# Kernel tuning notes

Hardware: AMD Instinct MI355X
Metric: run time of the kernel (lower is better)

## Reference

```python
import jax, jax.numpy as jnp
import numpy as np

N_NODES = 100000
N_EDGES = 1600000
IN_CH, HID_CH, N_CLASS = 512, 128, 40


def setup_inputs() -> dict:
    key = jax.random.key(0)
    k1, k2, k3, k4 = jax.random.split(key, 4)
    x = jax.random.normal(k1, (N_NODES, IN_CH), dtype=jnp.float32)
    edge_index = jax.random.randint(k2, (2, N_EDGES), 0, N_NODES, dtype=jnp.int64)
    W1 = jax.random.normal(k3, (IN_CH, HID_CH), dtype=jnp.float32) * (1.0 / np.sqrt(IN_CH))
    b1 = jnp.zeros((HID_CH,), dtype=jnp.float32)
    W2 = jax.random.normal(k4, (HID_CH, N_CLASS), dtype=jnp.float32) * (1.0 / np.sqrt(HID_CH))
    b2 = jnp.zeros((N_CLASS,), dtype=jnp.float32)
    return {"x": x, "edge_index": edge_index, "W1": W1, "b1": b1, "W2": W2, "b2": b2}


def _gcn_conv(x, src, dst, norm, W, b, n_nodes):
    # transform then sparse normalized aggregation: out = D^-1/2 (A+I) D^-1/2 (x W) + b
    h = x @ W                                  # [N, out_ch]
    msg = h[src] * norm[:, None]               # gather + scale, [E+N, out_ch]
    return jax.ops.segment_sum(msg, dst, num_segments=n_nodes) + b


def reference(x, edge_index, W1, b1, W2, b2):
    n = x.shape[0]
    loop = jnp.arange(n, dtype=edge_index.dtype)
    src = jnp.concatenate([edge_index[0], loop])   # add self-loops
    dst = jnp.concatenate([edge_index[1], loop])
    deg = jax.ops.segment_sum(jnp.ones_like(src, dtype=x.dtype), dst, num_segments=n)
    dinv = jnp.where(deg > 0, jax.lax.rsqrt(deg), 0.0)
    norm = dinv[src] * dinv[dst]                   # symmetric normalization

    h = jax.nn.relu(_gcn_conv(x, src, dst, norm, W1, b1, n))
    # dropout(p=0.5, train=False) -> identity in eval mode
    logits = _gcn_conv(h, src, dst, norm, W2, b2, n)
    return jax.nn.log_softmax(logits, axis=1)
```

## Files before the change

kernel.cpp:

```cpp
#include <hip/hip_runtime.h>
#include <math.h>

#define IN_CH 512
#define HID 128
#define NCLASS 40
#define SCAN_CHUNK 2048
#define FILL_CHUNKS 2048

typedef __attribute__((ext_vector_type(8))) short short8;
typedef __attribute__((ext_vector_type(4))) float float4v;

static __device__ inline ushort f2bf(float f) {
    unsigned int u = __float_as_uint(f);
    u += 0x7fffu + ((u >> 16) & 1u);
    return (ushort)(u >> 16);
}
static __device__ inline float bf2f(ushort u) {
    return __uint_as_float(((unsigned int)u) << 16);
}
static __device__ inline float blo(unsigned int u) { return __uint_as_float(u << 16); }
static __device__ inline float bhi(unsigned int u) { return __uint_as_float(u & 0xffff0000u); }

__global__ void k_count(const int* __restrict__ dst, int E, int* __restrict__ cnt) {
    int i = blockIdx.x * blockDim.x + threadIdx.x;
    if (i < E) atomicAdd(&cnt[dst[i]], 1);
}

__global__ __launch_bounds__(256) void k_scan_local(const int* __restrict__ cnt,
                                                    int* __restrict__ rowptr,
                                                    int* __restrict__ blocksum, int n) {
    __shared__ int ssum[256];
    int b = blockIdx.x, t = threadIdx.x;
    int base = b * SCAN_CHUNK + t * 8;
    int v[8], s = 0;
    #pragma unroll
    for (int i = 0; i < 8; ++i) {
        int idx = base + i;
        v[i] = (idx < n) ? cnt[idx] : 0;
        s += v[i];
    }
    ssum[t] = s;
    __syncthreads();
    for (int off = 1; off < 256; off <<= 1) {
        int x = (t >= off) ? ssum[t - off] : 0;
        __syncthreads();
        ssum[t] += x;
        __syncthreads();
    }
    int run = ssum[t] - s;
    #pragma unroll
    for (int i = 0; i < 8; ++i) {
        int idx = base + i;
        if (idx < n) rowptr[idx] = run;
        run += v[i];
    }
    if (t == 255) blocksum[b] = ssum[255];
}

__global__ void k_scan_blocksums(int* blocksum, int nb) {
    if (threadIdx.x == 0 && blockIdx.x == 0) {
        int acc = 0;
        for (int i = 0; i < nb; ++i) { int v = blocksum[i]; blocksum[i] = acc; acc += v; }
    }
}

__global__ void k_scan_add_dinv(int* __restrict__ rowptr, int* __restrict__ cursor,
                                const int* __restrict__ blocksum,
                                const int* __restrict__ cnt,
                                float* __restrict__ dinv, int n) {
    int i = blockIdx.x * blockDim.x + threadIdx.x;
    if (i < n) {
        int r = rowptr[i] + blocksum[i / SCAN_CHUNK];
        rowptr[i] = r;
        cursor[i] = r;
        dinv[i] = rsqrtf((float)cnt[i] + 1.0f);
    }
}

__global__ __launch_bounds__(256) void k_fill(const int* __restrict__ src,
                                              const int* __restrict__ dst,
                                              int* __restrict__ cursor,
                                              int* __restrict__ col, int E, int N) {
    int chunk = blockIdx.x;
    int e0 = (int)((long long)E * chunk / FILL_CHUNKS);
    int e1 = (int)((long long)E * (chunk + 1) / FILL_CHUNKS);
    int e = e0 + threadIdx.x;
    int s0 = 0, d0 = -1, s1 = 0, d1 = -1, s2 = 0, d2 = -1, s3 = 0, d3 = -1;
    if (e < e1)       { s0 = src[e];       d0 = dst[e]; }
    if (e + 256 < e1) { s1 = src[e + 256]; d1 = dst[e + 256]; }
    if (e + 512 < e1) { s2 = src[e + 512]; d2 = dst[e + 512]; }
    if (e + 768 < e1) { s3 = src[e + 768]; d3 = dst[e + 768]; }
    #pragma unroll
    for (int r = 0; r < 8; ++r) {
        int r0 = (N >> 3) * r;
        int r1 = (r == 7) ? N : r0 + (N >> 3);
        if (d0 >= r0 && d0 < r1) { int p = atomicAdd(&cursor[d0], 1); col[p] = s0; }
        if (d1 >= r0 && d1 < r1) { int p = atomicAdd(&cursor[d1], 1); col[p] = s1; }
        if (d2 >= r0 && d2 < r1) { int p = atomicAdd(&cursor[d2], 1); col[p] = s2; }
        if (d3 >= r0 && d3 < r1) { int p = atomicAdd(&cursor[d3], 1); col[p] = s3; }
    }
}

__global__ void k_wt(const float* __restrict__ W1, const float* __restrict__ W2,
                     ushort* __restrict__ W1t, ushort* __restrict__ W2t) {
    int i = blockIdx.x * blockDim.x + threadIdx.x;
    if (i < HID * IN_CH) {
        int n = i >> 9;
        int k = i & 511;
        W1t[i] = f2bf(W1[k * HID + n]);
    } else {
        int q = i - HID * IN_CH;
        int n = q >> 7;
        int k = q & 127;
        float v = (n < NCLASS) ? W2[k * NCLASS + n] : 0.f;
        W2t[q] = f2bf(v);
    }
}

#define GBM 128
#define GBK 64
#define KP 72
__global__ __launch_bounds__(256) void k_gemm1_mfma(const float* __restrict__ X,
                                                    const ushort* __restrict__ W1t,
                                                    const float* __restrict__ dinv,
                                                    ushort* __restrict__ H, int M) {
    __shared__ ushort As[GBM * KP];
    int t = threadIdx.x;
    int bm = blockIdx.x * GBM;
    int wave = t >> 6;
    int lane = t & 63;
    int m0w = (wave >> 1) * 64;
    int n0w = (wave & 1) * 64;
    int lrow = lane & 15;
    int quad = lane >> 4;

    float4v acc[4][4];
    #pragma unroll
    for (int i = 0; i < 4; ++i)
        #pragma unroll
        for (int j = 0; j < 4; ++j) acc[i][j] = (float4v)(0.f);

    int ar = t >> 1;
    int ah = (t & 1) * 32;
    int gmr = bm + ar;
    if (gmr >= M) gmr = M - 1;
    const float* gA = &X[(size_t)gmr * IN_CH + ah];

    float4 pre[8];
    #pragma unroll
    for (int i = 0; i < 8; ++i) pre[i] = *(const float4*)(gA + i * 4);

    for (int k0 = 0; k0 < IN_CH; k0 += GBK) {
        #pragma unroll
        for (int i = 0; i < 4; ++i) {
            union { ushort u[8]; uint4 v; } pk;
            float4 f0 = pre[2 * i], f1 = pre[2 * i + 1];
            pk.u[0] = f2bf(f0.x); pk.u[1] = f2bf(f0.y);
            pk.u[2] = f2bf(f0.z); pk.u[3] = f2bf(f0.w);
            pk.u[4] = f2bf(f1.x); pk.u[5] = f2bf(f1.y);
            pk.u[6] = f2bf(f1.z); pk.u[7] = f2bf(f1.w);
            *(uint4*)&As[ar * KP + ah + i * 8] = pk.v;
        }
        if (k0 + GBK < IN_CH) {
            #pragma unroll
            for (int i = 0; i < 8; ++i)
                pre[i] = *(const float4*)(gA + k0 + GBK + i * 4);
        }
        __syncthreads();
        #pragma unroll
        for (int kk = 0; kk < GBK; kk += 32) {
            short8 af[4], bfr[4];
            #pragma unroll
            for (int j = 0; j < 4; ++j)
                bfr[j] = *(const short8*)&W1t[(size_t)(n0w + j * 16 + lrow) * IN_CH
                                              + k0 + kk + quad * 8];
            #pragma unroll
            for (int i = 0; i < 4; ++i)
                af[i] = *(const short8*)&As[(m0w + i * 16 + lrow) * KP + kk + quad * 8];
            #pragma unroll
            for (int i = 0; i < 4; ++i)
                #pragma unroll
                for (int j = 0; j < 4; ++j)
                    acc[i][j] = __builtin_amdgcn_mfma_f32_16x16x32_bf16(
                        af[i], bfr[j], acc[i][j], 0, 0, 0);
        }
        __syncthreads();
    }
    #pragma unroll
    for (int i = 0; i < 4; ++i) {
        #pragma unroll
        for (int r = 0; r < 4; ++r) {
            int gm = bm + m0w + i * 16 + quad * 4 + r;
            if (gm < M) {
                float di = dinv[gm];
                #pragma unroll
                for (int j = 0; j < 4; ++j)
                    H[(size_t)gm * HID + n0w + j * 16 + lrow] = f2bf(acc[i][j][r] * di);
            }
        }
    }
}

__global__ __launch_bounds__(256) void k_agg1(const int* __restrict__ rowptr,
                                              const int* __restrict__ rowend,
                                              const int* __restrict__ col,
                                              const float* __restrict__ dinv,
                                              const unsigned int* __restrict__ h1b,
                                              const float* __restrict__ b1,
                                              unsigned int* __restrict__ hb, int N) {
    int wv = threadIdx.x >> 6;
    int t  = threadIdx.x & 63;
    int half = t >> 5;
    int l    = t & 31;
    int m = blockIdx.x * 4 + wv;
    if (m >= N) m = N - 1;
    float dm = dinv[m];
    float c0 = 0.f, c1 = 0.f, c2 = 0.f, c3 = 0.f;
    if (half == 0) {
        uint2 sv = *(const uint2*)&h1b[(size_t)m * 64 + 2 * l];
        c0 = blo(sv.x); c1 = bhi(sv.x); c2 = blo(sv.y); c3 = bhi(sv.y);
    }
    int j = rowptr[m], jend = rowend[m];
    for (; j + 8 <= jend; j += 8) {
        int sA = col[j + 0 + half];
        int sB = col[j + 2 + half];
        int sC = col[j + 4 + half];
        int sD = col[j + 6 + half];
        uint2 vA = *(const uint2*)&h1b[(size_t)sA * 64 + 2 * l];
        uint2 vB = *(const uint2*)&h1b[(size_t)sB * 64 + 2 * l];
        uint2 vC = *(const uint2*)&h1b[(size_t)sC * 64 + 2 * l];
        uint2 vD = *(const uint2*)&h1b[(size_t)sD * 64 + 2 * l];
        c0 += blo(vA.x); c1 += bhi(vA.x); c2 += blo(vA.y); c3 += bhi(vA.y);
        c0 += blo(vB.x); c1 += bhi(vB.x); c2 += blo(vB.y); c3 += bhi(vB.y);
        c0 += blo(vC.x); c1 += bhi(vC.x); c2 += blo(vC.y); c3 += bhi(vC.y);
        c0 += blo(vD.x); c1 += bhi(vD.x); c2 += blo(vD.y); c3 += bhi(vD.y);
    }
    for (; j + 2 <= jend; j += 2) {
        int s = col[j + half];
        uint2 v = *(const uint2*)&h1b[(size_t)s * 64 + 2 * l];
        c0 += blo(v.x); c1 += bhi(v.x); c2 += blo(v.y); c3 += bhi(v.y);
    }
    if (j < jend && half == 0) {
        int s = col[j];
        uint2 v = *(const uint2*)&h1b[(size_t)s * 64 + 2 * l];
        c0 += blo(v.x); c1 += bhi(v.x); c2 += blo(v.y); c3 += bhi(v.y);
    }
    c0 += __shfl_xor(c0, 32);
    c1 += __shfl_xor(c1, 32);
    c2 += __shfl_xor(c2, 32);
    c3 += __shfl_xor(c3, 32);
    if (half == 0) {
        float4 bb = *(const float4*)&b1[4 * l];
        float h0 = fmaxf(fmaf(c0, dm, bb.x), 0.f) * dm;
        float h1 = fmaxf(fmaf(c1, dm, bb.y), 0.f) * dm;
        float h2 = fmaxf(fmaf(c2, dm, bb.z), 0.f) * dm;
        float h3 = fmaxf(fmaf(c3, dm, bb.w), 0.f) * dm;
        uint2 o;
        o.x = (unsigned int)f2bf(h0) | ((unsigned int)f2bf(h1) << 16);
        o.y = (unsigned int)f2bf(h2) | ((unsigned int)f2bf(h3) << 16);
        *(uint2*)&hb[(size_t)m * 64 + 2 * l] = o;
    }
}

__global__ __launch_bounds__(256) void k_gemm2_mfma(const ushort* __restrict__ hb,
                                                    const ushort* __restrict__ W2t,
                                                    ushort* __restrict__ h2s, int M) {
    int t = threadIdx.x;
    int wave = t >> 6, lane = t & 63;
    int lrow = lane & 15, quad = lane >> 4;
    int row0 = blockIdx.x * 64 + wave * 16;
    int rm = row0 + lrow;
    if (rm >= M) rm = M - 1;
    const ushort* pa = &hb[(size_t)rm * HID + quad * 8];
    float4v acc[3];
    acc[0] = (float4v)(0.f); acc[1] = (float4v)(0.f); acc[2] = (float4v)(0.f);
    #pragma unroll
    for (int k0 = 0; k0 < HID; k0 += 32) {
        short8 a = *(const short8*)(pa + k0);
        #pragma unroll
        for (int jj = 0; jj < 3; ++jj) {
            short8 b = *(const short8*)&W2t[(size_t)(jj * 16 + lrow) * HID
                                            + k0 + quad * 8];
            acc[jj] = __builtin_amdgcn_mfma_f32_16x16x32_bf16(a, b, acc[jj], 0, 0, 0);
        }
    }
    #pragma unroll
    for (int jj = 0; jj < 3; ++jj) {
        int cls = jj * 16 + lrow;
        #pragma unroll
        for (int r = 0; r < 4; ++r) {
            int node = row0 + quad * 4 + r;
            if (node < M && cls < NCLASS)
                h2s[(size_t)node * NCLASS + cls] = f2bf(acc[jj][r]);
        }
    }
}

__global__ __launch_bounds__(256) void k_agg2_final(const int* __restrict__ rowptr,
                                                    const int* __restrict__ rowend,
                                                    const int* __restrict__ col,
                                                    const float* __restrict__ dinv,
                                                    const unsigned int* __restrict__ h2p,
                                                    const float* __restrict__ b2,
                                                    float* __restrict__ out, int N) {
    int wv = threadIdx.x >> 6;
    int t  = threadIdx.x & 63;
    int m = blockIdx.x * 4 + wv;
    if (m >= N) m = N - 1;
    float dm = dinv[m];
    int g = (t >= 40) ? 2 : ((t >= 20) ? 1 : 0);
    int u = t - g * 20;
    bool act = t < 60;
    float vx = 0.f, vy = 0.f;
    if (t < 20) {
        unsigned int v = h2p[(size_t)m * 20 + u];
        vx = blo(v);
        vy = bhi(v);
    }
    int j = rowptr[m] + g, jend = rowend[m];
    if (act) {
        for (; j + 3 < jend; j += 6) {
            int s0 = col[j], s1 = col[j + 3];
            unsigned int v0 = h2p[(size_t)s0 * 20 + u];
            unsigned int v1 = h2p[(size_t)s1 * 20 + u];
            vx += blo(v0); vy += bhi(v0);
            vx += blo(v1); vy += bhi(v1);
        }
        if (j < jend) {
            int s = col[j];
            unsigned int v = h2p[(size_t)s * 20 + u];
            vx += blo(v); vy += bhi(v);
        }
    }
    vx += __shfl(vx, t + 20) + __shfl(vx, t + 40);
    vy += __shfl(vy, t + 20) + __shfl(vy, t + 40);
    bool w = t < 20;
    float lx = 0.f, ly = 0.f;
    if (w) {
        float2 bb = ((const float2*)b2)[u];
        lx = fmaf(vx, dm, bb.x);
        ly = fmaf(vy, dm, bb.y);
    }
    float mv = w ? fmaxf(lx, ly) : -INFINITY;
    #pragma unroll
    for (int off = 32; off; off >>= 1) mv = fmaxf(mv, __shfl_xor(mv, off));
    float ex = w ? (expf(lx - mv) + expf(ly - mv)) : 0.f;
    #pragma unroll
    for (int off = 32; off; off >>= 1) ex += __shfl_xor(ex, off);
    float lse = mv + logf(ex);
    if (w) ((float2*)out)[(size_t)m * 20 + u] = make_float2(lx - lse, ly - lse);
}

extern "C" void kernel_launch(void* const* d_in, const int* in_sizes, int n_in,
                              void* d_out, int out_size, void* d_ws, size_t ws_size,
                              hipStream_t stream) {
    const float* x  = (const float*)d_in[0];
    const int*   ei = (const int*)d_in[1];
    const float* W1 = (const float*)d_in[2];
    const float* b1 = (const float*)d_in[3];
    const float* W2 = (const float*)d_in[4];
    const float* b2 = (const float*)d_in[5];
    float* out = (float*)d_out;

    const int N = in_sizes[0] / IN_CH;
    const int E = in_sizes[1] / 2;
    const int* src = ei;
    const int* dst = ei + E;

    const int NB_SCAN = (N + SCAN_CHUNK - 1) / SCAN_CHUNK;

    size_t Npad = ((size_t)N + 127) / 128 * 128;
    float* ws = (float*)d_ws;
    float* dinv    = ws;
    int*   cnt     = (int*)(ws + Npad);
    int*   rowptr  = (int*)(ws + 2 * Npad);
    int*   cursor  = (int*)(ws + 3 * Npad);
    int*   bsum    = (int*)(ws + 4 * Npad);
    int*   col     = (int*)(ws + 4 * Npad + 128);
    size_t o_h1    = 4 * Npad + 128 + (size_t)E;
    unsigned int* h1b = (unsigned int*)(ws + o_h1);
    unsigned int* hb  = (unsigned int*)(ws + o_h1 + (size_t)N * 64);
    unsigned int* h2p = (unsigned int*)(ws + o_h1 + (size_t)N * 128);
    ushort* W2t = (ushort*)(ws + o_h1 + (size_t)N * 148);
    ushort* W1t = (ushort*)h2p;

    hipMemsetAsync(cnt, 0, (size_t)N * sizeof(int), stream);
    k_count<<<(E + 255) / 256, 256, 0, stream>>>(dst, E, cnt);
    k_scan_local<<<NB_SCAN, 256, 0, stream>>>(cnt, rowptr, bsum, N);
    k_scan_blocksums<<<1, 64, 0, stream>>>(bsum, NB_SCAN);
    k_scan_add_dinv<<<(N + 255) / 256, 256, 0, stream>>>(rowptr, cursor, bsum,
                                                         cnt, dinv, N);
    k_fill<<<FILL_CHUNKS, 256, 0, stream>>>(src, dst, cursor, col, E, N);

    k_wt<<<(HID * IN_CH + 48 * HID) / 256, 256, 0, stream>>>(W1, W2, W1t, W2t);
    k_gemm1_mfma<<<(N + GBM - 1) / GBM, 256, 0, stream>>>(x, W1t, dinv,
                                                          (ushort*)h1b, N);
    k_agg1<<<(N + 3) / 4, 256, 0, stream>>>(rowptr, cursor, col, dinv,
                                            h1b, b1, hb, N);

    k_gemm2_mfma<<<(N + 63) / 64, 256, 0, stream>>>((const ushort*)hb, W2t,
                                                    (ushort*)h2p, N);
    k_agg2_final<<<(N + 3) / 4, 256, 0, stream>>>(rowptr, cursor, col, dinv,
                                                  h2p, b2, out, N);
}
```

Before: 643.6 us.

## Slice layer-1 aggregation across feature columns and split CSR fill by dst range

The CSR fill kernel now launches eight times as many blocks, each handling one destination-node range for its edge chunk, instead of one block looping over all eight ranges. This spreads the atomics over more blocks but reads each edge's dst eight times. The layer-1 aggregation is split into eight column slices of 16 features, with 16 edges handled in parallel per wave (4 lanes per edge) and a shuffle reduction at the end. The slicing is meant to improve cache locality on gathered rows and add parallelism for low-degree nodes, at the cost of re-reading col indices eight times and more blocks.

```diff
diff --git a/kernel.cpp b/kernel.cpp
--- a/kernel.cpp
+++ b/kernel.cpp
@@ -81,23 +81,18 @@
                                               const int* __restrict__ dst,
                                               int* __restrict__ cursor,
                                               int* __restrict__ col, int E, int N) {
-    int chunk = blockIdx.x;
+    int range = blockIdx.x & 7;
+    int chunk = blockIdx.x >> 3;
+    int r0 = (N >> 3) * range;
+    int r1 = (range == 7) ? N : r0 + (N >> 3);
     int e0 = (int)((long long)E * chunk / FILL_CHUNKS);
     int e1 = (int)((long long)E * (chunk + 1) / FILL_CHUNKS);
-    int e = e0 + threadIdx.x;
-    int s0 = 0, d0 = -1, s1 = 0, d1 = -1, s2 = 0, d2 = -1, s3 = 0, d3 = -1;
-    if (e < e1)       { s0 = src[e];       d0 = dst[e]; }
-    if (e + 256 < e1) { s1 = src[e + 256]; d1 = dst[e + 256]; }
-    if (e + 512 < e1) { s2 = src[e + 512]; d2 = dst[e + 512]; }
-    if (e + 768 < e1) { s3 = src[e + 768]; d3 = dst[e + 768]; }
-    #pragma unroll
-    for (int r = 0; r < 8; ++r) {
-        int r0 = (N >> 3) * r;
-        int r1 = (r == 7) ? N : r0 + (N >> 3);
-        if (d0 >= r0 && d0 < r1) { int p = atomicAdd(&cursor[d0], 1); col[p] = s0; }
-        if (d1 >= r0 && d1 < r1) { int p = atomicAdd(&cursor[d1], 1); col[p] = s1; }
-        if (d2 >= r0 && d2 < r1) { int p = atomicAdd(&cursor[d2], 1); col[p] = s2; }
-        if (d3 >= r0 && d3 < r1) { int p = atomicAdd(&cursor[d3], 1); col[p] = s3; }
+    for (int e = e0 + threadIdx.x; e < e1; e += 256) {
+        int d = dst[e];
+        if (d >= r0 && d < r1) {
+            int p = atomicAdd(&cursor[d], 1);
+            col[p] = src[e];
+        }
     }
 }
 
@@ -201,56 +196,42 @@
     }
 }
 
-__global__ __launch_bounds__(256) void k_agg1(const int* __restrict__ rowptr,
-                                              const int* __restrict__ rowend,
-                                              const int* __restrict__ col,
-                                              const float* __restrict__ dinv,
-                                              const unsigned int* __restrict__ h1b,
-                                              const float* __restrict__ b1,
-                                              unsigned int* __restrict__ hb, int N) {
+__global__ __launch_bounds__(1024) void k_agg1_slice(const int* __restrict__ rowptr,
+                                                     const int* __restrict__ rowend,
+                                                     const int* __restrict__ col,
+                                                     const float* __restrict__ dinv,
+                                                     const unsigned int* __restrict__ h1b,
+                                                     const float* __restrict__ b1,
+                                                     unsigned int* __restrict__ hb, int N) {
+    int slice = blockIdx.x & 7;
     int wv = threadIdx.x >> 6;
-    int t  = threadIdx.x & 63;
-    int half = t >> 5;
-    int l    = t & 31;
-    int m = blockIdx.x * 4 + wv;
+    int lane = threadIdx.x & 63;
+    int g  = lane >> 2;
+    int il = lane & 3;
+    int m = (blockIdx.x >> 3) * 16 + wv;
     if (m >= N) m = N - 1;
-    float dm = dinv[m];
+    int boff = slice * 8 + il * 2;
     float c0 = 0.f, c1 = 0.f, c2 = 0.f, c3 = 0.f;
-    if (half == 0) {
-        uint2 sv = *(const uint2*)&h1b[(size_t)m * 64 + 2 * l];
-        c0 = blo(sv.x); c1 = bhi(sv.x); c2 = blo(sv.y); c3 = bhi(sv.y);
-    }
-    int j = rowptr[m], jend = rowend[m];
-    for (; j + 8 <= jend; j += 8) {
-        int sA = col[j + 0 + half];
-        int sB = col[j + 2 + half];
-        int sC = col[j + 4 + half];
-        int sD = col[j + 6 + half];
-        uint2 vA = *(const uint2*)&h1b[(size_t)sA * 64 + 2 * l];
-        uint2 vB = *(const uint2*)&h1b[(size_t)sB * 64 + 2 * l];
-        uint2 vC = *(const uint2*)&h1b[(size_t)sC * 64 + 2 * l];
-        uint2 vD = *(const uint2*)&h1b[(size_t)sD * 64 + 2 * l];
-        c0 += blo(vA.x); c1 += bhi(vA.x); c2 += blo(vA.y); c3 += bhi(vA.y);
-        c0 += blo(vB.x); c1 += bhi(vB.x); c2 += blo(vB.y); c3 += bhi(vB.y);
-        c0 += blo(vC.x); c1 += bhi(vC.x); c2 += blo(vC.y); c3 += bhi(vC.y);
-        c0 += blo(vD.x); c1 += bhi(vD.x); c2 += blo(vD.y); c3 += bhi(vD.y);
-    }
-    for (; j + 2 <= jend; j += 2) {
-        int s = col[j + half];
-        uint2 v = *(const uint2*)&h1b[(size_t)s * 64 + 2 * l];
-        c0 += blo(v.x); c1 += bhi(v.x); c2 += blo(v.y); c3 += bhi(v.y);
-    }
-    if (j < jend && half == 0) {
-        int s = col[j];
-        uint2 v = *(const uint2*)&h1b[(size_t)s * 64 + 2 * l];
-        c0 += blo(v.x); c1 += bhi(v.x); c2 += blo(v.y); c3 += bhi(v.y);
-    }
-    c0 += __shfl_xor(c0, 32);
-    c1 += __shfl_xor(c1, 32);
-    c2 += __shfl_xor(c2, 32);
-    c3 += __shfl_xor(c3, 32);
-    if (half == 0) {
-        float4 bb = *(const float4*)&b1[4 * l];
+    int j0 = rowptr[m], jend = rowend[m];
+    int jv = jend + 1;
+    for (int j = j0; j < jv; j += 16) {
+        int jg = j + g;
+        if (jg < jv) {
+            int s = (jg < jend) ? col[jg] : m;
+            uint2 v = *(const uint2*)&h1b[(size_t)s * 64 + boff];
+            c0 += blo(v.x); c1 += bhi(v.x); c2 += blo(v.y); c3 += bhi(v.y);
+        }
+    }
+    #pragma unroll
+    for (int off = 4; off < 64; off <<= 1) {
+        c0 += __shfl_xor(c0, off);
+        c1 += __shfl_xor(c1, off);
+        c2 += __shfl_xor(c2, off);
+        c3 += __shfl_xor(c3, off);
+    }
+    if (g == 0) {
+        float dm = dinv[m];
+        float4 bb = *(const float4*)&b1[slice * 16 + il * 4];
         float h0 = fmaxf(fmaf(c0, dm, bb.x), 0.f) * dm;
         float h1 = fmaxf(fmaf(c1, dm, bb.y), 0.f) * dm;
         float h2 = fmaxf(fmaf(c2, dm, bb.z), 0.f) * dm;
@@ -258,7 +239,7 @@
         uint2 o;
         o.x = (unsigned int)f2bf(h0) | ((unsigned int)f2bf(h1) << 16);
         o.y = (unsigned int)f2bf(h2) | ((unsigned int)f2bf(h3) << 16);
-        *(uint2*)&hb[(size_t)m * 64 + 2 * l] = o;
+        *(uint2*)&hb[(size_t)m * 64 + boff] = o;
     }
 }
 
@@ -390,13 +371,13 @@
     k_scan_blocksums<<<1, 64, 0, stream>>>(bsum, NB_SCAN);
     k_scan_add_dinv<<<(N + 255) / 256, 256, 0, stream>>>(rowptr, cursor, bsum,
                                                          cnt, dinv, N);
-    k_fill<<<FILL_CHUNKS, 256, 0, stream>>>(src, dst, cursor, col, E, N);
+    k_fill<<<8 * FILL_CHUNKS, 256, 0, stream>>>(src, dst, cursor, col, E, N);
 
     k_wt<<<(HID * IN_CH + 48 * HID) / 256, 256, 0, stream>>>(W1, W2, W1t, W2t);
     k_gemm1_mfma<<<(N + GBM - 1) / GBM, 256, 0, stream>>>(x, W1t, dinv,
                                                           (ushort*)h1b, N);
-    k_agg1<<<(N + 3) / 4, 256, 0, stream>>>(rowptr, cursor, col, dinv,
-                                            h1b, b1, hb, N);
+    k_agg1_slice<<<8 * ((N + 15) / 16), 1024, 0, stream>>>(rowptr, cursor, col,
+                                                           dinv, h1b, b1, hb, N);
 
     k_gemm2_mfma<<<(N + 63) / 64, 256, 0, stream>>>((const ushort*)hb, W2t,
                                                     (ushort*)h2p, N);
```

New measurement: 849.2 us. 32.0% more time.
